# Performance work log

Hardware: AMD Instinct MI355X
Metric: run time of the kernel (lower is better)

Reference implementation:

```python
import jax, jax.numpy as jnp
import numpy as np

# Production-scale dims (GraspNet-style CloudCrop)
B, N, C, NS = 8, 1024, 256, 32          # batch, seed points (= npoint), feat dim, nsample
RADIUS, HMIN, HMAX = 0.05, -0.02, 0.04
EPS = 1e-5


def setup_inputs() -> dict:
    key = jax.random.key(0)
    ks = jax.random.split(key, 8)
    # seed points in a 0.2m cube -> cylinder of r=0.05, h=0.06 holds ~60 pts on avg
    seed_xyz_graspable = jax.random.uniform(ks[0], (B, N, 3), dtype=jnp.float32) * 0.2
    seed_features_graspable = jax.random.normal(ks[1], (B, C, N), dtype=jnp.float32)
    # random proper-ish rotation matrices via batched QR (orthonormal columns)
    q, _ = jnp.linalg.qr(jax.random.normal(ks[2], (B, N, 3, 3), dtype=jnp.float32))
    vp_rot = q
    cin = 3 + C
    # kaiming_normal for 1x1 convs (fan_in = cin), BN -> no conv bias
    W1 = jax.random.normal(ks[3], (256, cin), dtype=jnp.float32) * np.sqrt(2.0 / cin)
    W2 = jax.random.normal(ks[4], (256, 256), dtype=jnp.float32) * np.sqrt(2.0 / 256)
    g1 = jnp.ones((256,), jnp.float32); b1 = jnp.zeros((256,), jnp.float32)
    g2 = jnp.ones((256,), jnp.float32); b2 = jnp.zeros((256,), jnp.float32)
    return dict(seed_xyz_graspable=seed_xyz_graspable,
                seed_features_graspable=seed_features_graspable,
                vp_rot=vp_rot, W1=W1, g1=g1, b1=b1, W2=W2, g2=g2, b2=b2)


def _cylinder_query_idx(xyz, new_xyz, rot):
    # local coords: x_rot = R^T (p - c); rot flattened row-major in the original,
    # so local_k = sum_m rot[m, k] * diff_m  ==  einsum(diff, rot)
    diff = xyz[:, None, :, :] - new_xyz[:, :, None, :]          # (B, P, N, 3)
    local = jnp.einsum('bpnm,bpmk->bpnk', diff, rot)            # (B, P, N, 3)
    d2 = local[..., 1] ** 2 + local[..., 2] ** 2
    mask = (d2 < RADIUS ** 2) & (local[..., 0] > HMIN) & (local[..., 0] < HMAX)
    # first NS in-cylinder indices in original point order; empty slots -> index 0
    order = jnp.argsort(~mask, axis=-1)[..., :NS]               # stable sort
    valid = jnp.take_along_axis(mask, order, axis=-1)
    return jnp.where(valid, order, 0)                           # (B, P, NS) int32


def _conv_bn_relu(x, W, g, b):
    # 1x1 conv as channel GEMM, BatchNorm2d (training stats), ReLU
    y = jnp.einsum('bcps,oc->bops', x, W)                       # (B, O, P, S)
    mu = y.mean(axis=(0, 2, 3), keepdims=True)
    var = y.var(axis=(0, 2, 3), keepdims=True)
    y = (y - mu) * jax.lax.rsqrt(var + EPS)
    y = y * g[None, :, None, None] + b[None, :, None, None]
    return jax.nn.relu(y)


def reference(seed_xyz_graspable, seed_features_graspable, vp_rot,
              W1, g1, b1, W2, g2, b2):
    xyz, feats, rot = seed_xyz_graspable, seed_features_graspable, vp_rot
    idx = _cylinder_query_idx(xyz, xyz, rot)                    # centers == seeds
    # group xyz: gather, recenter, normalize by radius, rotate into cylinder frame
    gx = jax.vmap(lambda p, i: p[i])(xyz, idx)                  # (B, P, NS, 3)
    gx = (gx - xyz[:, :, None, :]) / RADIUS
    gx = jnp.einsum('bpsm,bpmk->bpsk', gx, rot)                 # rotate_xyz
    gf = jax.vmap(lambda f, i: f[:, i])(feats, idx)             # (B, C, P, NS)
    x = jnp.concatenate([gx.transpose(0, 3, 1, 2), gf], axis=1)  # (B, 3+C, P, NS)
    x = _conv_bn_relu(x, W1, g1, b1)
    x = _conv_bn_relu(x, W2, g2, b2)
    return x.max(axis=-1)                                        # (B, 256, P)
```

## Files before the change

kernel.cpp:

```cpp
#include <hip/hip_runtime.h>
#include <hip/hip_bf16.h>

#define DB 8
#define DN 1024
#define DP 1024
#define DC 256
#define DNS 32
#define DBP (DB * DP)
#define K1 288
#define K2 256
#define XS 296
#define YS 258
#define ROWS 128
#define NG (DBP / 4)
#define NK1 (K1 / 32)
#define NK2 (K2 / 32)
#define NSL 32

constexpr float kRadius = 0.05f;
constexpr float kR2 = kRadius * kRadius;
constexpr float kHmin = -0.02f;
constexpr float kHmax = 0.04f;
constexpr float kEps = 1e-5f;
constexpr float kInvCnt = 1.0f / (float)(DB * DP * DNS);

typedef __bf16 bf16x8 __attribute__((ext_vector_type(8)));
typedef float f32x4 __attribute__((ext_vector_type(4)));
static_assert(sizeof(bf16x8) == 16, "bf16x8 must be 16B");

constexpr size_t OF_FEATST = 0;
constexpr size_t OF_W1B  = OF_FEATST + (size_t)DB * DN * DC / 2;
constexpr size_t OF_W2B  = OF_W1B + (size_t)DC * K1 / 2;
constexpr size_t OF_IDX  = OF_W2B + (size_t)DC * K2 / 2;
constexpr size_t OF_GX   = OF_IDX + (size_t)DBP * DNS;
constexpr size_t OF_PART = OF_GX + (size_t)DBP * DNS * 3;
constexpr size_t OF_YMAX = OF_PART + (size_t)NG * DC * 2;
constexpr size_t OF_YMIN = OF_YMAX + (size_t)DBP * DC / 2;
constexpr size_t OF_BN1  = OF_YMIN + (size_t)DBP * DC / 2;
constexpr size_t OF_BN2  = OF_BN1 + 512;
constexpr size_t OF_CNTZ = OF_PART;
constexpr size_t OF_GWZ  = OF_CNTZ + (size_t)256 * DN;
constexpr size_t OF_GG   = OF_GWZ + (size_t)256 * 3 * DN;
constexpr size_t OF_YPRT = OF_GG + 4096;

__device__ inline ushort f2b(float x) {
  union { __hip_bfloat16 h; ushort u; } c;
  c.h = __float2bfloat16(x);
  return c.u;
}
__device__ inline float b2f(ushort u) {
  union { uint u; float f; } c;
  c.u = (uint)u << 16;
  return c.f;
}

__global__ __launch_bounds__(256)
void k_prep(const float* __restrict__ f, uint* __restrict__ ftb,
            const float* __restrict__ W1, ushort* __restrict__ W1b,
            const float* __restrict__ W2, ushort* __restrict__ W2b,
            const float* __restrict__ xyz, const float* __restrict__ rot,
            int* __restrict__ idxp, float* __restrict__ gxp) {
  __shared__ float t[32][33];
  __shared__ int sidx[4][DNS];
  __shared__ float srot[4][9], sc[4][3];
  int blk = blockIdx.x;
  int tid = threadIdx.x;
  if (blk < 2048) {
    int ct = blk & 7, nt = (blk >> 3) & 31, b = blk >> 8;
    int tx = tid & 31, ty = tid >> 5;
#pragma unroll
    for (int k = 0; k < 4; ++k) {
      int c = ct * 32 + ty + k * 8;
      t[ty + k * 8][tx] = f[((size_t)b * DC + c) * DN + nt * 32 + tx];
    }
    __syncthreads();
    uint* dst = ftb + (size_t)b * DN * (DC / 2);
#pragma unroll
    for (int it = 0; it < 2; ++it) {
      int idx = it * 256 + tid;
      int nl = idx >> 4, cp = idx & 15;
      uint v = (uint)f2b(t[2 * cp][nl]) | ((uint)f2b(t[2 * cp + 1][nl]) << 16);
      dst[(size_t)(nt * 32 + nl) * (DC / 2) + ct * 16 + cp] = v;
    }
  } else if (blk < 2336) {
    int gid = (blk - 2048) * 256 + tid;
    if (gid < DC * K1) {
      int o = gid / K1, kp = gid - o * K1;
      float v = 0.f;
      if (kp < 256) v = W1[o * 259 + 3 + kp];
      else if (kp < 259) v = W1[o * 259 + (kp - 256)];
      W1b[gid] = f2b(v);
    }
  } else if (blk < 2592) {
    int gid = (blk - 2336) * 256 + tid;
    if (gid < DC * K2) W2b[gid] = f2b(W2[gid]);
  } else {
    int wv = tid >> 6;
    int lane = tid & 63;
    int bp = (blk - 2592) * 4 + wv;
    int b = bp >> 10;
    if (lane < DNS) sidx[wv][lane] = 0;
    if (lane < 9) srot[wv][lane] = rot[(size_t)bp * 9 + lane];
    if (lane < 3) sc[wv][lane] = xyz[(size_t)bp * 3 + lane];
    float r00 = srot[wv][0], r01 = srot[wv][1], r02 = srot[wv][2];
    float r10 = srot[wv][3], r11 = srot[wv][4], r12 = srot[wv][5];
    float r20 = srot[wv][6], r21 = srot[wv][7], r22 = srot[wv][8];
    float cx = sc[wv][0], cy = sc[wv][1], cz = sc[wv][2];
    const float* xb = xyz + (size_t)b * DN * 3;
    int cnt = 0;
    for (int ch = 0; ch < DN / 64 && cnt < DNS; ++ch) {
      int n = ch * 64 + lane;
      float dx = xb[n * 3 + 0] - cx, dy = xb[n * 3 + 1] - cy, dz = xb[n * 3 + 2] - cz;
      float lx = dx * r00 + dy * r10 + dz * r20;
      float ly = dx * r01 + dy * r11 + dz * r21;
      float lz = dx * r02 + dy * r12 + dz * r22;
      bool m = (ly * ly + lz * lz < kR2) && (lx > kHmin) && (lx < kHmax);
      unsigned long long bal = __ballot(m);
      int rank = cnt + __popcll(bal & ((1ull << lane) - 1ull));
      if (m && rank < DNS) sidx[wv][rank] = n;
      cnt += __popcll(bal);
    }
    if (lane < DNS) {
      int j = sidx[wv][lane];
      idxp[(size_t)bp * DNS + lane] = j;
      float gx = (xb[j * 3 + 0] - cx) / kRadius;
      float gy = (xb[j * 3 + 1] - cy) / kRadius;
      float gz = (xb[j * 3 + 2] - cz) / kRadius;
      float* gp = gxp + ((size_t)bp * DNS + lane) * 3;
      gp[0] = gx * r00 + gy * r10 + gz * r20;
      gp[1] = gx * r01 + gy * r11 + gz * r21;
      gp[2] = gx * r02 + gy * r12 + gz * r22;
    }
  }
}

__global__ __launch_bounds__(256)
void k_count(const int* __restrict__ idxp, const float* __restrict__ gxp,
             float* __restrict__ cntz, float* __restrict__ gwz,
             float* __restrict__ gg) {
  __shared__ float h0[DN], h1[DN], h2[DN], h3[DN];
  int t = threadIdx.x;
  int blk = blockIdx.x;
  for (int i = t; i < DN; i += 256) {
    h0[i] = 0.f; h1[i] = 0.f; h2[i] = 0.f; h3[i] = 0.f;
  }
  __syncthreads();
  float p[9] = {0.f, 0.f, 0.f, 0.f, 0.f, 0.f, 0.f, 0.f, 0.f};
#pragma unroll
  for (int r = 0; r < 4; ++r) {
    int sid = blk * 1024 + r * 256 + t;
    int j = idxp[sid];
    const float* g = gxp + (size_t)sid * 3;
    float g0 = g[0], g1 = g[1], g2 = g[2];
    atomicAdd(&h0[j], 1.f);
    atomicAdd(&h1[j], g0);
    atomicAdd(&h2[j], g1);
    atomicAdd(&h3[j], g2);
    p[0] += g0 * g0; p[1] += g0 * g1; p[2] += g0 * g2;
    p[3] += g1 * g1; p[4] += g1 * g2; p[5] += g2 * g2;
    p[6] += g0; p[7] += g1; p[8] += g2;
  }
  __syncthreads();
  for (int i = t; i < DN; i += 256) {
    cntz[(size_t)blk * DN + i] = h0[i];
    gwz[((size_t)blk * 3 + 0) * DN + i] = h1[i];
    gwz[((size_t)blk * 3 + 1) * DN + i] = h2[i];
    gwz[((size_t)blk * 3 + 2) * DN + i] = h3[i];
  }
  __shared__ float sgg[4][9];
#pragma unroll
  for (int v = 0; v < 9; ++v) {
    float sv = p[v];
#pragma unroll
    for (int m = 1; m < 64; m <<= 1) sv += __shfl_xor(sv, m, 64);
    if ((t & 63) == 0) sgg[t >> 6][v] = sv;
  }
  __syncthreads();
  if (t < 9) gg[blk * 16 + t] = sgg[0][t] + sgg[1][t] + sgg[2][t] + sgg[3][t];
}

__global__ __launch_bounds__(256)
void k_ygemm(const uint4* __restrict__ ftb, const ushort* __restrict__ W1b,
             const float* __restrict__ W1, const float* __restrict__ cntz,
             const float* __restrict__ gwz, float2* __restrict__ ypart) {
  __shared__ ushort x_lds[ROWS * XS];
  __shared__ float c_lds[ROWS];
  __shared__ float g_lds[3][ROWS];
  __shared__ float wg_lds[DC][3];

  const int nb = blockIdx.x;
  const int row = nb >> 2;
  const int oq = nb & 3;
  const int b = row >> 3;
  const int n0 = (row & 7) * ROWS;
  const int tid = threadIdx.x;
  const int lane = tid & 63;
  const int wv = tid >> 6;
  const int l15 = lane & 15;
  const int l4 = lane >> 4;

  {
    const uint4* src = ftb + ((size_t)b * DN + n0) * (DC / 8);
    for (int idx = tid; idx < ROWS * 32; idx += 256) {
      int rrow = idx >> 5, col = idx & 31;
      ((uint4*)(x_lds + (size_t)rrow * XS))[col] = src[rrow * 32 + col];
    }
  }
  if (tid < ROWS) {
    float c = 0.f, g0 = 0.f, g1 = 0.f, g2 = 0.f;
    for (int s = 0; s < NSL; ++s) {
      int blk = b * NSL + s;
      c += cntz[(size_t)blk * DN + n0 + tid];
      g0 += gwz[((size_t)blk * 3 + 0) * DN + n0 + tid];
      g1 += gwz[((size_t)blk * 3 + 1) * DN + n0 + tid];
      g2 += gwz[((size_t)blk * 3 + 2) * DN + n0 + tid];
    }
    c_lds[tid] = c; g_lds[0][tid] = g0; g_lds[1][tid] = g1; g_lds[2][tid] = g2;
  }
  {
    wg_lds[tid][0] = W1[tid * 259 + 0];
    wg_lds[tid][1] = W1[tid * 259 + 1];
    wg_lds[tid][2] = W1[tid * 259 + 2];
  }
  __syncthreads();

  f32x4 acc[8];
#pragma unroll
  for (int st = 0; st < 8; ++st)
#pragma unroll
    for (int r = 0; r < 4; ++r) acc[st][r] = 0.f;

  const int o0 = oq * 64 + wv * 16;
  const ushort* xbase = x_lds + (size_t)l15 * XS + l4 * 8;
  {
    const ushort* wrow = W1b + (size_t)(o0 + l15) * K1 + l4 * 8;
#pragma unroll
    for (int ks = 0; ks < 8; ++ks) {
      bf16x8 bx[8];
#pragma unroll
      for (int st = 0; st < 8; ++st)
        bx[st] = *(const bf16x8*)(xbase + (size_t)st * 16 * XS + ks * 32);
      bf16x8 aw = *(const bf16x8*)(wrow + ks * 32);
#pragma unroll
      for (int st = 0; st < 8; ++st)
        acc[st] = __builtin_amdgcn_mfma_f32_16x16x32_bf16(aw, bx[st],
                                                          acc[st], 0, 0, 0);
    }
  }

  float cn[8], h0[8], h1[8], h2[8];
#pragma unroll
  for (int st = 0; st < 8; ++st) {
    int n = st * 16 + l15;
    cn[st] = c_lds[n]; h0[st] = g_lds[0][n]; h1[st] = g_lds[1][n]; h2[st] = g_lds[2][n];
  }
#pragma unroll
  for (int r = 0; r < 4; ++r) {
    int o = o0 + l4 * 4 + r;
    float wg0 = wg_lds[o][0], wg1 = wg_lds[o][1], wg2 = wg_lds[o][2];
    float s = 0.f, q = 0.f;
#pragma unroll
    for (int st = 0; st < 8; ++st) {
      float Y = acc[st][r];
      float h = wg0 * h0[st] + wg1 * h1[st] + wg2 * h2[st];
      s = fmaf(cn[st], Y, s);
      q += cn[st] * Y * Y + 2.f * Y * h;
    }
#pragma unroll
    for (int m = 1; m < 16; m <<= 1) {
      s += __shfl_xor(s, m, 64);
      q += __shfl_xor(q, m, 64);
    }
    if (l15 == 0) ypart[(size_t)row * DC + o] = make_float2(s, q);
  }
}

__global__ __launch_bounds__(256)
void k_bn1f(const float2* __restrict__ ypart, const float* __restrict__ gg,
            const float* __restrict__ W1, const float* __restrict__ gam,
            const float* __restrict__ bet, float* __restrict__ bn) {
  __shared__ float ggs[9];
  int t = threadIdx.x;
  if (t < 9) {
    float s = 0.f;
    for (int blk = 0; blk < 256; ++blk) s += gg[blk * 16 + t];
    ggs[t] = s;
  }
  __syncthreads();
  float s = 0.f, q = 0.f;
  for (int nb = 0; nb < 64; ++nb) {
    float2 v = ypart[(size_t)nb * DC + t];
    s += v.x; q += v.y;
  }
  float wg0 = W1[t * 259 + 0], wg1 = W1[t * 259 + 1], wg2 = W1[t * 259 + 2];
  s += wg0 * ggs[6] + wg1 * ggs[7] + wg2 * ggs[8];
  q += wg0 * wg0 * ggs[0] + 2.f * wg0 * wg1 * ggs[1] + 2.f * wg0 * wg2 * ggs[2] +
       wg1 * wg1 * ggs[3] + 2.f * wg1 * wg2 * ggs[4] + wg2 * wg2 * ggs[5];
  float mu = s * kInvCnt;
  float var = q * kInvCnt - mu * mu;
  var = var < 0.f ? 0.f : var;
  float sc = gam[t] * rsqrtf(var + kEps);
  bn[t] = sc;
  bn[DC + t] = bet[t] - mu * sc;
}

__global__ __launch_bounds__(512, 4)
void k_gemm_full(const uint4* __restrict__ ftb, const ushort* __restrict__ W1b,
                 const ushort* __restrict__ W2b, const int* __restrict__ idxp,
                 const float* __restrict__ gxp, const float* __restrict__ bn1,
                 float2* __restrict__ part, ushort* __restrict__ ymax,
                 ushort* __restrict__ ymin) {
  __shared__ ushort x_lds[ROWS * XS];
  __shared__ float bn_lds[2 * DC];

  const int bid = blockIdx.x;
  const int grp = (bid & 7) * (NG / 8) + (bid >> 3);
  const int bp0 = grp * 4;
  const int b = bp0 >> 10;
  const int tid = threadIdx.x;
  const int lane = tid & 63;
  const int wv = tid >> 6;
  const int l15 = lane & 15;
  const int l4 = lane >> 4;

  bn_lds[tid] = bn1[tid];

  {
    int q = tid & 7;
#pragma unroll
    for (int rep = 0; rep < 2; ++rep) {
      int s = (tid >> 3) + rep * 64;
      int j = idxp[(size_t)bp0 * DNS + s];
      const uint4* src = ftb + (size_t)(b * DN + j) * (DC / 8);
      uint4* dst = (uint4*)(x_lds + (size_t)s * XS);
#pragma unroll
      for (int k = 0; k < 4; ++k) dst[q + 8 * k] = src[q + 8 * k];
    }
  }
  if (tid < ROWS) {
    const float* g = gxp + ((size_t)bp0 * DNS + tid) * 3;
    uint a0 = (uint)f2b(g[0]) | ((uint)f2b(g[1]) << 16);
    uint a1 = (uint)f2b(g[2]);
    uint4* drow = (uint4*)(x_lds + (size_t)tid * XS + 256);
    drow[0] = make_uint4(a0, a1, 0u, 0u);
    drow[1] = make_uint4(0u, 0u, 0u, 0u);
    drow[2] = make_uint4(0u, 0u, 0u, 0u);
    drow[3] = make_uint4(0u, 0u, 0u, 0u);
  }
  __syncthreads();

  f32x4 acc[2][8];
#pragma unroll
  for (int t = 0; t < 2; ++t)
#pragma unroll
    for (int st = 0; st < 8; ++st)
#pragma unroll
      for (int r = 0; r < 4; ++r) acc[t][st][r] = 0.f;

  const int o0 = wv * 32;
  const ushort* xbase = x_lds + (size_t)l15 * XS + l4 * 8;

  {
    const ushort* wrow[2];
#pragma unroll
    for (int t = 0; t < 2; ++t)
      wrow[t] = W1b + (size_t)(o0 + t * 16 + l15) * K1 + l4 * 8;
    bf16x8 aw[2];
#pragma unroll
    for (int t = 0; t < 2; ++t) aw[t] = *(const bf16x8*)(wrow[t]);
#pragma unroll
    for (int ks = 0; ks < NK1; ++ks) {
      bf16x8 bx[8];
#pragma unroll
      for (int st = 0; st < 8; ++st)
        bx[st] = *(const bf16x8*)(xbase + (size_t)st * 16 * XS + ks * 32);
      bf16x8 an[2];
      if (ks + 1 < NK1) {
#pragma unroll
        for (int t = 0; t < 2; ++t)
          an[t] = *(const bf16x8*)(wrow[t] + (ks + 1) * 32);
      }
      __builtin_amdgcn_s_setprio(1);
#pragma unroll
      for (int st = 0; st < 8; ++st)
#pragma unroll
        for (int t = 0; t < 2; ++t)
          acc[t][st] = __builtin_amdgcn_mfma_f32_16x16x32_bf16(aw[t], bx[st],
                                                               acc[t][st], 0, 0, 0);
      __builtin_amdgcn_s_setprio(0);
      if (ks + 1 < NK1) {
#pragma unroll
        for (int t = 0; t < 2; ++t) aw[t] = an[t];
      }
    }
  }

  __syncthreads();
#pragma unroll
  for (int t = 0; t < 2; ++t) {
    int ob = o0 + t * 16 + l4 * 4;
    float sc0 = bn_lds[ob + 0], sh0 = bn_lds[DC + ob + 0];
    float sc1 = bn_lds[ob + 1], sh1 = bn_lds[DC + ob + 1];
    float sc2 = bn_lds[ob + 2], sh2 = bn_lds[DC + ob + 2];
    float sc3 = bn_lds[ob + 3], sh3 = bn_lds[DC + ob + 3];
#pragma unroll
    for (int st = 0; st < 8; ++st) {
      float v0 = fmaxf(fmaf(acc[t][st][0], sc0, sh0), 0.f);
      float v1 = fmaxf(fmaf(acc[t][st][1], sc1, sh1), 0.f);
      float v2 = fmaxf(fmaf(acc[t][st][2], sc2, sh2), 0.f);
      float v3 = fmaxf(fmaf(acc[t][st][3], sc3, sh3), 0.f);
      uint2 pk = make_uint2((uint)f2b(v0) | ((uint)f2b(v1) << 16),
                            (uint)f2b(v2) | ((uint)f2b(v3) << 16));
      int s = st * 16 + l15;
      *(uint2*)(x_lds + (size_t)s * XS + ob) = pk;
      acc[t][st][0] = 0.f; acc[t][st][1] = 0.f;
      acc[t][st][2] = 0.f; acc[t][st][3] = 0.f;
    }
  }
  __syncthreads();

  {
    const ushort* wrow[2];
#pragma unroll
    for (int t = 0; t < 2; ++t)
      wrow[t] = W2b + (size_t)(o0 + t * 16 + l15) * K2 + l4 * 8;
    bf16x8 aw[2];
#pragma unroll
    for (int t = 0; t < 2; ++t) aw[t] = *(const bf16x8*)(wrow[t]);
#pragma unroll
    for (int ks = 0; ks < NK2; ++ks) {
      bf16x8 bx[8];
#pragma unroll
      for (int st = 0; st < 8; ++st)
        bx[st] = *(const bf16x8*)(xbase + (size_t)st * 16 * XS + ks * 32);
      bf16x8 an[2];
      if (ks + 1 < NK2) {
#pragma unroll
        for (int t = 0; t < 2; ++t)
          an[t] = *(const bf16x8*)(wrow[t] + (ks + 1) * 32);
      }
      __builtin_amdgcn_s_setprio(1);
#pragma unroll
      for (int st = 0; st < 8; ++st)
#pragma unroll
        for (int t = 0; t < 2; ++t)
          acc[t][st] = __builtin_amdgcn_mfma_f32_16x16x32_bf16(aw[t], bx[st],
                                                               acc[t][st], 0, 0, 0);
      __builtin_amdgcn_s_setprio(0);
      if (ks + 1 < NK2) {
#pragma unroll
        for (int t = 0; t < 2; ++t) aw[t] = an[t];
      }
    }
  }

  __syncthreads();
#pragma unroll
  for (int t = 0; t < 2; ++t) {
    int ob = o0 + t * 16 + l4 * 4;
#pragma unroll
    for (int st = 0; st < 8; ++st) {
      uint2 pk = make_uint2(
          (uint)f2b(acc[t][st][0]) | ((uint)f2b(acc[t][st][1]) << 16),
          (uint)f2b(acc[t][st][2]) | ((uint)f2b(acc[t][st][3]) << 16));
      int s = st * 16 + l15;
      *(uint2*)(x_lds + (size_t)s * YS + ob) = pk;
    }
  }
  __syncthreads();
  {
    float* redp = (float*)(x_lds + (size_t)ROWS * YS);
    int o = tid & 255, half = tid >> 8;
    const ushort* col = x_lds + o;
    float s = 0.f, q = 0.f;
#pragma unroll
    for (int p2 = 0; p2 < 2; ++p2) {
      int p = half * 2 + p2;
      float mx = -3.4e38f, mn = 3.4e38f;
#pragma unroll 8
      for (int i = 0; i < DNS; ++i) {
        float v = b2f(col[(size_t)(p * DNS + i) * YS]);
        s += v; q += v * v;
        mx = fmaxf(mx, v); mn = fminf(mn, v);
      }
      ymax[(size_t)(bp0 + p) * DC + o] = f2b(mx);
      ymin[(size_t)(bp0 + p) * DC + o] = f2b(mn);
    }
    redp[half * 256 + o] = s;
    redp[512 + half * 256 + o] = q;
    __syncthreads();
    if (tid < 256) {
      float ss = redp[tid] + redp[256 + tid];
      float qq = redp[512 + tid] + redp[768 + tid];
      part[(size_t)grp * DC + tid] = make_float2(ss, qq);
    }
  }
}

__global__ void k_reduce_bn(const float* __restrict__ part, const float* __restrict__ gam,
                            const float* __restrict__ bet, float* __restrict__ bn) {
  int o = blockIdx.x, tid = threadIdx.x;
  __shared__ float ss[256], sq[256];
  float s = 0.f, q = 0.f;
  const float2* pp = (const float2*)part;
  for (int g = tid; g < NG; g += 256) {
    float2 v = pp[(size_t)g * DC + o];
    s += v.x; q += v.y;
  }
  ss[tid] = s; sq[tid] = q;
  __syncthreads();
  for (int w = 128; w > 0; w >>= 1) {
    if (tid < w) { ss[tid] += ss[tid + w]; sq[tid] += sq[tid + w]; }
    __syncthreads();
  }
  if (tid == 0) {
    float mu = ss[0] * kInvCnt;
    float var = sq[0] * kInvCnt - mu * mu;
    var = var < 0.f ? 0.f : var;
    float sc = gam[o] * rsqrtf(var + kEps);
    bn[o] = sc;
    bn[DC + o] = bet[o] - mu * sc;
  }
}

__global__ void k_final(const ushort* __restrict__ ymax, const ushort* __restrict__ ymin,
                        const float* __restrict__ bn2, float* __restrict__ out) {
  __shared__ float tmax[32][33], tmin[32][33];
  int ot = blockIdx.x, pt = blockIdx.y, b = blockIdx.z;
  int tx = threadIdx.x, ty = threadIdx.y;
#pragma unroll
  for (int k = 0; k < 4; ++k) {
    int pr = ty + k * 8;
    size_t base = ((size_t)(b * DP) + pt * 32 + pr) * DC + ot * 32 + tx;
    tmax[pr][tx] = b2f(ymax[base]);
    tmin[pr][tx] = b2f(ymin[base]);
  }
  __syncthreads();
#pragma unroll
  for (int k = 0; k < 4; ++k) {
    int oc = ty + k * 8;
    int o = ot * 32 + oc;
    float sc = bn2[o], sh = bn2[DC + o];
    float m = (sc >= 0.f) ? tmax[tx][oc] : tmin[tx][oc];
    float v = fmaf(sc, m, sh);
    v = v > 0.f ? v : 0.f;
    out[((size_t)(b * DC) + o) * DP + pt * 32 + tx] = v;
  }
}

extern "C" void kernel_launch(void* const* d_in, const int* in_sizes, int n_in,
                              void* d_out, int out_size, void* d_ws, size_t ws_size,
                              hipStream_t stream) {
  const float* xyz   = (const float*)d_in[0];
  const float* feats = (const float*)d_in[1];
  const float* rot   = (const float*)d_in[2];
  const float* W1    = (const float*)d_in[3];
  const float* g1    = (const float*)d_in[4];
  const float* b1    = (const float*)d_in[5];
  const float* W2    = (const float*)d_in[6];
  const float* g2    = (const float*)d_in[7];
  const float* b2    = (const float*)d_in[8];
  float* out = (float*)d_out;

  float* ws = (float*)d_ws;
  uint*   ftb_u  = (uint*)(ws + OF_FEATST);
  uint4*  ftb    = (uint4*)(ws + OF_FEATST);
  ushort* W1b    = (ushort*)(ws + OF_W1B);
  ushort* W2b    = (ushort*)(ws + OF_W2B);
  int*    idxp   = (int*)(ws + OF_IDX);
  float*  gxp    = ws + OF_GX;
  float2* partp  = (float2*)(ws + OF_PART);
  ushort* ymaxp  = (ushort*)(ws + OF_YMAX);
  ushort* yminp  = (ushort*)(ws + OF_YMIN);
  float*  bn1p   = ws + OF_BN1;
  float*  bn2p   = ws + OF_BN2;
  float*  cntzp  = ws + OF_CNTZ;
  float*  gwzp   = ws + OF_GWZ;
  float*  ggp    = ws + OF_GG;
  float2* yprtp  = (float2*)(ws + OF_YPRT);

  k_prep<<<4640, 256, 0, stream>>>(feats, ftb_u, W1, W1b, W2, W2b,
                                   xyz, rot, idxp, gxp);

  k_count<<<256, 256, 0, stream>>>(idxp, gxp, cntzp, gwzp, ggp);
  k_ygemm<<<256, 256, 0, stream>>>(ftb, W1b, W1, cntzp, gwzp, yprtp);
  k_bn1f<<<1, 256, 0, stream>>>(yprtp, ggp, W1, g1, b1, bn1p);

  k_gemm_full<<<NG, 512, 0, stream>>>(ftb, W1b, W2b, idxp, gxp, bn1p, partp,
                                      ymaxp, yminp);
  k_reduce_bn<<<DC, 256, 0, stream>>>((const float*)partp, g2, b2, bn2p);
  k_final<<<dim3(DC / 32, DP / 32, DB), dim3(32, 8), 0, stream>>>(ymaxp, yminp, bn2p, out);
}
```

Measured before the change: 141.3 us.

## Reuse per-point layer-1 GEMM output instead of recomputing it per grouped sample

Layer 1 is linear, so the feature part of the first conv is computed once per source point in k_ygemm (W1·feat[n]) and stored as bf16. k_gemm_full then gathers these precomputed rows by neighbor index and adds the xyz contribution through folded BN-scaled weights (sc*W1[:,0..2]) before ReLU. This removes the first GEMM over the 32x-expanded grouped tensor inside k_gemm_full. The cost is an extra bf16 global buffer write and read, plus one more bf16 rounding of the pre-BN activations.

Result: no change. 140.8 us (-0.3%).

```diff
diff --git a/kernel.cpp b/kernel.cpp
--- a/kernel.cpp
+++ b/kernel.cpp
@@ -10,10 +10,10 @@
 #define K1 288
 #define K2 256
 #define XS 296
+#define XS2 264
 #define YS 258
 #define ROWS 128
 #define NG (DBP / 4)
-#define NK1 (K1 / 32)
 #define NK2 (K2 / 32)
 #define NSL 32
 
@@ -37,7 +37,8 @@
 constexpr size_t OF_YMAX = OF_PART + (size_t)NG * DC * 2;
 constexpr size_t OF_YMIN = OF_YMAX + (size_t)DBP * DC / 2;
 constexpr size_t OF_BN1  = OF_YMIN + (size_t)DBP * DC / 2;
-constexpr size_t OF_BN2  = OF_BN1 + 512;
+constexpr size_t OF_BN2  = OF_BN1 + 1536;
+constexpr size_t OF_YFB  = OF_BN2 + 512;
 constexpr size_t OF_CNTZ = OF_PART;
 constexpr size_t OF_GWZ  = OF_CNTZ + (size_t)256 * DN;
 constexpr size_t OF_GG   = OF_GWZ + (size_t)256 * 3 * DN;
@@ -182,7 +183,8 @@
 __global__ __launch_bounds__(256)
 void k_ygemm(const uint4* __restrict__ ftb, const ushort* __restrict__ W1b,
              const float* __restrict__ W1, const float* __restrict__ cntz,
-             const float* __restrict__ gwz, float2* __restrict__ ypart) {
+             const float* __restrict__ gwz, float2* __restrict__ ypart,
+             ushort* __restrict__ yfb) {
   __shared__ ushort x_lds[ROWS * XS];
   __shared__ float c_lds[ROWS];
   __shared__ float g_lds[3][ROWS];
@@ -248,6 +250,15 @@
     }
   }
 
+#pragma unroll
+  for (int st = 0; st < 8; ++st) {
+    uint2 pk = make_uint2(
+        (uint)f2b(acc[st][0]) | ((uint)f2b(acc[st][1]) << 16),
+        (uint)f2b(acc[st][2]) | ((uint)f2b(acc[st][3]) << 16));
+    int n = n0 + st * 16 + l15;
+    *(uint2*)(yfb + ((size_t)b * DN + n) * DC + o0 + l4 * 4) = pk;
+  }
+
   float cn[8], h0[8], h1[8], h2[8];
 #pragma unroll
   for (int st = 0; st < 8; ++st) {
@@ -302,16 +313,19 @@
   float sc = gam[t] * rsqrtf(var + kEps);
   bn[t] = sc;
   bn[DC + t] = bet[t] - mu * sc;
+  bn[2 * DC + t] = sc * wg0;
+  bn[3 * DC + t] = sc * wg1;
+  bn[4 * DC + t] = sc * wg2;
 }
 
 __global__ __launch_bounds__(512, 4)
-void k_gemm_full(const uint4* __restrict__ ftb, const ushort* __restrict__ W1b,
-                 const ushort* __restrict__ W2b, const int* __restrict__ idxp,
-                 const float* __restrict__ gxp, const float* __restrict__ bn1,
-                 float2* __restrict__ part, ushort* __restrict__ ymax,
-                 ushort* __restrict__ ymin) {
-  __shared__ ushort x_lds[ROWS * XS];
-  __shared__ float bn_lds[2 * DC];
+void k_gemm_full(const ushort* __restrict__ yfb, const ushort* __restrict__ W2b,
+                 const int* __restrict__ idxp, const float* __restrict__ gxp,
+                 const float* __restrict__ bn1, float2* __restrict__ part,
+                 ushort* __restrict__ ymax, ushort* __restrict__ ymin) {
+  __shared__ ushort x_lds[ROWS * XS2];
+  __shared__ float bnp[5 * DC];
+  __shared__ float redp[1024];
 
   const int bid = blockIdx.x;
   const int grp = (bid & 7) * (NG / 8) + (bid >> 3);
@@ -323,29 +337,49 @@
   const int l15 = lane & 15;
   const int l4 = lane >> 4;
 
-  bn_lds[tid] = bn1[tid];
+  for (int i = tid; i < 5 * DC; i += 512) bnp[i] = bn1[i];
+  __syncthreads();
 
   {
-    int q = tid & 7;
-#pragma unroll
-    for (int rep = 0; rep < 2; ++rep) {
-      int s = (tid >> 3) + rep * 64;
-      int j = idxp[(size_t)bp0 * DNS + s];
-      const uint4* src = ftb + (size_t)(b * DN + j) * (DC / 8);
-      uint4* dst = (uint4*)(x_lds + (size_t)s * XS);
-#pragma unroll
-      for (int k = 0; k < 4; ++k) dst[q + 8 * k] = src[q + 8 * k];
-    }
-  }
-  if (tid < ROWS) {
-    const float* g = gxp + ((size_t)bp0 * DNS + tid) * 3;
-    uint a0 = (uint)f2b(g[0]) | ((uint)f2b(g[1]) << 16);
-    uint a1 = (uint)f2b(g[2]);
-    uint4* drow = (uint4*)(x_lds + (size_t)tid * XS + 256);
-    drow[0] = make_uint4(a0, a1, 0u, 0u);
-    drow[1] = make_uint4(0u, 0u, 0u, 0u);
-    drow[2] = make_uint4(0u, 0u, 0u, 0u);
-    drow[3] = make_uint4(0u, 0u, 0u, 0u);
+    int s = tid >> 2, q = tid & 3;
+    int j = idxp[(size_t)bp0 * DNS + s];
+    const float* g = gxp + ((size_t)bp0 * DNS + s) * 3;
+    float g0 = g[0], g1 = g[1], g2 = g[2];
+    const uint4* yfr = (const uint4*)(yfb + ((size_t)b * DN + j) * DC) + q * 8;
+    ushort* drow = x_lds + (size_t)s * XS2 + q * 64;
+#pragma unroll
+    for (int c = 0; c < 8; ++c) {
+      uint4 v = yfr[c];
+      int ob = q * 64 + c * 8;
+      float4 scA = *(const float4*)&bnp[ob];
+      float4 scB = *(const float4*)&bnp[ob + 4];
+      float4 shA = *(const float4*)&bnp[DC + ob];
+      float4 shB = *(const float4*)&bnp[DC + ob + 4];
+      float4 w0A = *(const float4*)&bnp[2 * DC + ob];
+      float4 w0B = *(const float4*)&bnp[2 * DC + ob + 4];
+      float4 w1A = *(const float4*)&bnp[3 * DC + ob];
+      float4 w1B = *(const float4*)&bnp[3 * DC + ob + 4];
+      float4 w2A = *(const float4*)&bnp[4 * DC + ob];
+      float4 w2B = *(const float4*)&bnp[4 * DC + ob + 4];
+      float y0 = b2f((ushort)(v.x & 0xffff)), y1 = b2f((ushort)(v.x >> 16));
+      float y2 = b2f((ushort)(v.y & 0xffff)), y3 = b2f((ushort)(v.y >> 16));
+      float y4 = b2f((ushort)(v.z & 0xffff)), y5 = b2f((ushort)(v.z >> 16));
+      float y6 = b2f((ushort)(v.w & 0xffff)), y7 = b2f((ushort)(v.w >> 16));
+      float r0 = fmaxf(fmaf(scA.x, y0, fmaf(w0A.x, g0, fmaf(w1A.x, g1, fmaf(w2A.x, g2, shA.x)))), 0.f);
+      float r1 = fmaxf(fmaf(scA.y, y1, fmaf(w0A.y, g0, fmaf(w1A.y, g1, fmaf(w2A.y, g2, shA.y)))), 0.f);
+      float r2 = fmaxf(fmaf(scA.z, y2, fmaf(w0A.z, g0, fmaf(w1A.z, g1, fmaf(w2A.z, g2, shA.z)))), 0.f);
+      float r3 = fmaxf(fmaf(scA.w, y3, fmaf(w0A.w, g0, fmaf(w1A.w, g1, fmaf(w2A.w, g2, shA.w)))), 0.f);
+      float r4 = fmaxf(fmaf(scB.x, y4, fmaf(w0B.x, g0, fmaf(w1B.x, g1, fmaf(w2B.x, g2, shB.x)))), 0.f);
+      float r5 = fmaxf(fmaf(scB.y, y5, fmaf(w0B.y, g0, fmaf(w1B.y, g1, fmaf(w2B.y, g2, shB.y)))), 0.f);
+      float r6 = fmaxf(fmaf(scB.z, y6, fmaf(w0B.z, g0, fmaf(w1B.z, g1, fmaf(w2B.z, g2, shB.z)))), 0.f);
+      float r7 = fmaxf(fmaf(scB.w, y7, fmaf(w0B.w, g0, fmaf(w1B.w, g1, fmaf(w2B.w, g2, shB.w)))), 0.f);
+      uint4 pk;
+      pk.x = (uint)f2b(r0) | ((uint)f2b(r1) << 16);
+      pk.y = (uint)f2b(r2) | ((uint)f2b(r3) << 16);
+      pk.z = (uint)f2b(r4) | ((uint)f2b(r5) << 16);
+      pk.w = (uint)f2b(r6) | ((uint)f2b(r7) << 16);
+      *(uint4*)(drow + c * 8) = pk;
+    }
   }
   __syncthreads();
 
@@ -358,66 +392,7 @@
       for (int r = 0; r < 4; ++r) acc[t][st][r] = 0.f;
 
   const int o0 = wv * 32;
-  const ushort* xbase = x_lds + (size_t)l15 * XS + l4 * 8;
-
-  {
-    const ushort* wrow[2];
-#pragma unroll
-    for (int t = 0; t < 2; ++t)
-      wrow[t] = W1b + (size_t)(o0 + t * 16 + l15) * K1 + l4 * 8;
-    bf16x8 aw[2];
-#pragma unroll
-    for (int t = 0; t < 2; ++t) aw[t] = *(const bf16x8*)(wrow[t]);
-#pragma unroll
-    for (int ks = 0; ks < NK1; ++ks) {
-      bf16x8 bx[8];
-#pragma unroll
-      for (int st = 0; st < 8; ++st)
-        bx[st] = *(const bf16x8*)(xbase + (size_t)st * 16 * XS + ks * 32);
-      bf16x8 an[2];
-      if (ks + 1 < NK1) {
-#pragma unroll
-        for (int t = 0; t < 2; ++t)
-          an[t] = *(const bf16x8*)(wrow[t] + (ks + 1) * 32);
-      }
-      __builtin_amdgcn_s_setprio(1);
-#pragma unroll
-      for (int st = 0; st < 8; ++st)
-#pragma unroll
-        for (int t = 0; t < 2; ++t)
-          acc[t][st] = __builtin_amdgcn_mfma_f32_16x16x32_bf16(aw[t], bx[st],
-                                                               acc[t][st], 0, 0, 0);
-      __builtin_amdgcn_s_setprio(0);
-      if (ks + 1 < NK1) {
-#pragma unroll
-        for (int t = 0; t < 2; ++t) aw[t] = an[t];
-      }
-    }
-  }
-
-  __syncthreads();
-#pragma unroll
-  for (int t = 0; t < 2; ++t) {
-    int ob = o0 + t * 16 + l4 * 4;
-    float sc0 = bn_lds[ob + 0], sh0 = bn_lds[DC + ob + 0];
-    float sc1 = bn_lds[ob + 1], sh1 = bn_lds[DC + ob + 1];
-    float sc2 = bn_lds[ob + 2], sh2 = bn_lds[DC + ob + 2];
-    float sc3 = bn_lds[ob + 3], sh3 = bn_lds[DC + ob + 3];
-#pragma unroll
-    for (int st = 0; st < 8; ++st) {
-      float v0 = fmaxf(fmaf(acc[t][st][0], sc0, sh0), 0.f);
-      float v1 = fmaxf(fmaf(acc[t][st][1], sc1, sh1), 0.f);
-      float v2 = fmaxf(fmaf(acc[t][st][2], sc2, sh2), 0.f);
-      float v3 = fmaxf(fmaf(acc[t][st][3], sc3, sh3), 0.f);
-      uint2 pk = make_uint2((uint)f2b(v0) | ((uint)f2b(v1) << 16),
-                            (uint)f2b(v2) | ((uint)f2b(v3) << 16));
-      int s = st * 16 + l15;
-      *(uint2*)(x_lds + (size_t)s * XS + ob) = pk;
-      acc[t][st][0] = 0.f; acc[t][st][1] = 0.f;
-      acc[t][st][2] = 0.f; acc[t][st][3] = 0.f;
-    }
-  }
-  __syncthreads();
+  const ushort* xbase = x_lds + (size_t)l15 * XS2 + l4 * 8;
 
   {
     const ushort* wrow[2];
@@ -432,7 +407,7 @@
       bf16x8 bx[8];
 #pragma unroll
       for (int st = 0; st < 8; ++st)
-        bx[st] = *(const bf16x8*)(xbase + (size_t)st * 16 * XS + ks * 32);
+        bx[st] = *(const bf16x8*)(xbase + (size_t)st * 16 * XS2 + ks * 32);
       bf16x8 an[2];
       if (ks + 1 < NK2) {
 #pragma unroll
@@ -469,7 +444,6 @@
   }
   __syncthreads();
   {
-    float* redp = (float*)(x_lds + (size_t)ROWS * YS);
     int o = tid & 255, half = tid >> 8;
     const ushort* col = x_lds + o;
     float s = 0.f, q = 0.f;
@@ -574,6 +548,7 @@
   ushort* yminp  = (ushort*)(ws + OF_YMIN);
   float*  bn1p   = ws + OF_BN1;
   float*  bn2p   = ws + OF_BN2;
+  ushort* yfbp   = (ushort*)(ws + OF_YFB);
   float*  cntzp  = ws + OF_CNTZ;
   float*  gwzp   = ws + OF_GWZ;
   float*  ggp    = ws + OF_GG;
@@ -583,10 +558,10 @@
                                    xyz, rot, idxp, gxp);
 
   k_count<<<256, 256, 0, stream>>>(idxp, gxp, cntzp, gwzp, ggp);
-  k_ygemm<<<256, 256, 0, stream>>>(ftb, W1b, W1, cntzp, gwzp, yprtp);
+  k_ygemm<<<256, 256, 0, stream>>>(ftb, W1b, W1, cntzp, gwzp, yprtp, yfbp);
   k_bn1f<<<1, 256, 0, stream>>>(yprtp, ggp, W1, g1, b1, bn1p);
 
-  k_gemm_full<<<NG, 512, 0, stream>>>(ftb, W1b, W2b, idxp, gxp, bn1p, partp,
+  k_gemm_full<<<NG, 512, 0, stream>>>(yfbp, W2b, idxp, gxp, bn1p, partp,
                                       ymaxp, yminp);
   k_reduce_bn<<<DC, 256, 0, stream>>>((const float*)partp, g2, b2, bn2p);
   k_final<<<dim3(DC / 32, DP / 32, DB), dim3(32, 8), 0, stream>>>(ymaxp, yminp, bn2p, out);
```
